# Performance work log

Hardware: AMD Instinct MI355X
Metric: run time of the kernel (lower is better)

## Reference

```python
import jax, jax.numpy as jnp
import numpy as np

E = 1024
BUCKET = 16
TAU = 0.75
ITERS = 8
SCALE = E ** -0.5
EPS = 1e-6


def _gumbel(rng, shape):
    u = jax.random.uniform(rng, shape, jnp.float32, 0.0, 1.0)
    return -jnp.log(-jnp.log(u + EPS) + EPS)


def _log_sinkhorn(log_alpha, n_iter):
    def body(i, la):
        la = la - jax.scipy.special.logsumexp(la, axis=-1, keepdims=True)
        la = la - jax.scipy.special.logsumexp(la, axis=-2, keepdims=True)
        return la
    return jnp.exp(jax.lax.fori_loop(0, n_iter, body, log_alpha))


def setup_inputs() -> dict:
    rng = jax.random.key(0)
    ks = jax.random.split(rng, 9)
    T, B, S = 4096, 8, 4096
    w = 0.02
    return {
        "query": jax.random.normal(ks[0], (T, B, E), jnp.float32),
        "key": jax.random.normal(ks[1], (S, B, E), jnp.float32),
        "value": jax.random.normal(ks[2], (S, B, E), jnp.float32),
        "wq": jax.random.normal(ks[3], (E, E), jnp.float32) * w,
        "bq": jnp.zeros((E,), jnp.float32),
        "wk": jax.random.normal(ks[4], (E, E), jnp.float32) * w,
        "bk": jnp.zeros((E,), jnp.float32),
        "wo": jax.random.normal(ks[5], (E, E), jnp.float32) * w,
        "bo": jnp.zeros((E,), jnp.float32),
    }


def reference(query, key, value, wq, bq, wk, bk, wo, bo):
    T, B, _ = query.shape
    S = key.shape[0]
    # projections (Linear: x @ W.T + b), move to (B, T, E)
    q = jnp.einsum('tbe,fe->btf', query, wq) + bq
    k = jnp.einsum('sbe,fe->bsf', key, wk) + bk
    v = jnp.transpose(value, (1, 0, 2))  # (B, S, E)
    nb, nkb = T // BUCKET, S // BUCKET
    # bucket aggregation: mean-pool q/k, flatten v buckets
    qb = q.reshape(B, nb, BUCKET, E).mean(axis=2)          # (B, nb, E)
    kb = k.reshape(B, nkb, BUCKET, E).mean(axis=2)         # (B, nkb, E)
    vb = v.reshape(B, nkb, BUCKET * E)                     # (B, nkb, BUCKET*E)
    # dot energy
    logits = jnp.einsum('bqe,bke->bqk', qb, kb) * SCALE    # (B, nb, nkb)
    log_alpha = logits
    # gumbel-sinkhorn (noise=True)
    g = _gumbel(jax.random.key(42), logits.shape)
    attn_weights = _log_sinkhorn((logits.astype(jnp.float32) + g) / TAU, ITERS)
    # attend on flattened buckets, then un-aggregate
    attn = jnp.einsum('bqk,bkd->bqd', attn_weights, vb)    # (B, nb, BUCKET*E)
    attn = attn.reshape(B, nb * BUCKET, E)
    attn = jnp.transpose(attn, (1, 0, 2))                  # (T, B, E)
    out = jnp.einsum('tbe,fe->tbf', attn, wo) + bo
    return out, attn_weights, log_alpha
```

## Files before the change

### kernel.cpp

```cpp
#include <hip/hip_runtime.h>


typedef float    f32x4 __attribute__((ext_vector_type(4)));
typedef _Float16 h4    __attribute__((ext_vector_type(4)));
typedef _Float16 h8    __attribute__((ext_vector_type(8)));

#define OUT_ELEMS 33554432
#define AW_ELEMS  524288

__device__ __forceinline__ void gload16(const void* g, void* l) {
  __builtin_amdgcn_global_load_lds((__attribute__((address_space(1))) void*)g,
                                   (__attribute__((address_space(3))) void*)l,
                                   16, 0, 0);
}

__global__ __launch_bounds__(256) void convw_k(const float* __restrict__ wq,
                                               const float* __restrict__ wk,
                                               const float* __restrict__ wo,
                                               _Float16* __restrict__ dst) {
  int which = blockIdx.y;
  const float* src = which == 0 ? wq : (which == 1 ? wk : wo);
  size_t idx = (size_t)blockIdx.x * 256 + threadIdx.x;
  f32x4 v = ((const f32x4*)src)[idx];
  ((h4*)(dst + (size_t)which * 1048576))[idx] = __builtin_convertvector(v, h4);
}

__global__ __launch_bounds__(256) void bucket_k(const float* __restrict__ q,
                                                const float* __restrict__ k,
                                                _Float16* __restrict__ qbar,
                                                _Float16* __restrict__ kbar) {
  const float* src = blockIdx.y ? k : q;
  _Float16* dst = blockIdx.y ? kbar : qbar;
  unsigned t = blockIdx.x * 256 + threadIdx.x;
  int e4 = t & 255, i = (t >> 8) & 255, b = t >> 16;
  const f32x4* p = (const f32x4*)(src + ((size_t)(i * 16) * 8 + b) * 1024) + e4;
  f32x4 acc = {0.f, 0.f, 0.f, 0.f};
  #pragma unroll
  for (int j = 0; j < 16; ++j) acc += p[j * 2048];
  acc *= 0.0625f;
  ((h4*)(dst + (size_t)(b * 256 + i) * 1024))[e4] = __builtin_convertvector(acc, h4);
}

__global__ __launch_bounds__(256) void vtrans_k(const float* __restrict__ v,
                                                _Float16* __restrict__ vt) {
  int bid = blockIdx.x;
  int kb = bid & 3, eb = (bid >> 2) & 15, j = (bid >> 6) & 15, b = bid >> 10;
  int k0 = kb * 64, e0 = eb * 64;
  __shared__ _Float16 tile[64][72];
  int t = threadIdx.x, r = t >> 2, qq = t & 3;
  const float* src = v + ((size_t)((k0 + r) * 16 + j) * 8 + b) * 1024 + e0;
  #pragma unroll
  for (int ii = 0; ii < 4; ++ii) {
    f32x4 x = ((const f32x4*)src)[qq + ii * 4];
    *(h4*)&tile[r][(qq + ii * 4) * 4] = __builtin_convertvector(x, h4);
  }
  __syncthreads();
  _Float16* dstp = vt + (((size_t)(b * 16 + j) * 1024 + e0 + r) * 256 + k0 + qq * 16);
  h8 o0, o1;
  #pragma unroll
  for (int kk = 0; kk < 8; ++kk) o0[kk] = tile[qq * 16 + kk][r];
  #pragma unroll
  for (int kk = 0; kk < 8; ++kk) o1[kk] = tile[qq * 16 + 8 + kk][r];
  *(h8*)dstp = o0;
  *(h8*)(dstp + 8) = o1;
}

__device__ __forceinline__ unsigned rotl32(unsigned x, int r) {
  return (x << r) | (x >> (32 - r));
}
__global__ __launch_bounds__(256) void gumbel_k(const float* __restrict__ logits,
                                                float* __restrict__ ebuf) {
  unsigned i = blockIdx.x * 256 + threadIdx.x;
  const unsigned k0 = 0u, k1 = 42u, k2 = 0u ^ 42u ^ 0x1BD11BDAu;
  unsigned x0 = 0u + k0, x1 = i + k1;
#define R4(a,b,c,d) \
  x0 += x1; x1 = rotl32(x1, a); x1 ^= x0; \
  x0 += x1; x1 = rotl32(x1, b); x1 ^= x0; \
  x0 += x1; x1 = rotl32(x1, c); x1 ^= x0; \
  x0 += x1; x1 = rotl32(x1, d); x1 ^= x0;
  R4(13,15,26,6)  x0 += k1; x1 += k2 + 1u;
  R4(17,29,16,24) x0 += k2; x1 += k0 + 2u;
  R4(13,15,26,6)  x0 += k0; x1 += k1 + 3u;
  R4(17,29,16,24) x0 += k1; x1 += k2 + 4u;
  R4(13,15,26,6)  x0 += k2; x1 += k0 + 5u;
#undef R4
  unsigned bits = x0 ^ x1;
  float u = __builtin_bit_cast(float, (bits >> 9) | 0x3f800000u) - 1.0f;
  float g = -logf(-logf(u + 1e-6f) + 1e-6f);
  ebuf[i] = __expf((logits[i] + g) / 0.75f);
}

__global__ __launch_bounds__(1024) void sink_rc_k(const float* __restrict__ ein,
                                                  float* __restrict__ attnw,
                                                  _Float16* __restrict__ wsh) {
  const int b = blockIdx.x;
  const int t = threadIdx.x;
  const int r = t >> 2, p = t & 3;
  const int k = t & 255, g = t >> 8;
  const float* Eb = ein + (size_t)b * 65536;
  const f32x4* Eb4 = (const f32x4*)Eb;

  __shared__ float ra[256];
  __shared__ float cb[256];
  __shared__ float part[4][256];
  if (t < 256) cb[t] = 1.0f;
  __syncthreads();

  const f32x4* cb4 = (const f32x4*)cb;

  for (int it = 0; it < 8; ++it) {
    float s = 0.f;
    #pragma unroll
    for (int i = 0; i < 16; ++i) {
      f32x4 e = Eb4[r * 64 + p * 16 + i];
      f32x4 c = cb4[p * 16 + i];
      f32x4 m = e * c;
      s += (m[0] + m[1]) + (m[2] + m[3]);
    }
    s += __shfl_xor(s, 1, 64);
    s += __shfl_xor(s, 2, 64);
    if (p == 0) ra[r] = 1.0f / s;
    __syncthreads();
    float s2 = 0.f;
    #pragma unroll 8
    for (int q2 = 0; q2 < 64; ++q2) {
      int row = g * 64 + q2;
      s2 += Eb[row * 256 + k] * ra[row];
    }
    part[g][k] = s2;
    __syncthreads();
    if (t < 256) {
      cb[t] = 1.0f / (part[0][t] + part[1][t] + part[2][t] + part[3][t]);
    }
    __syncthreads();
  }

  const float arow = ra[r];
  f32x4* aw = (f32x4*)(attnw + (size_t)b * 65536 + r * 256 + p * 64);
  h4* wh = (h4*)(wsh + (size_t)b * 65536 + r * 256 + p * 64);
  #pragma unroll
  for (int i = 0; i < 16; ++i) {
    f32x4 e = Eb4[r * 64 + p * 16 + i];
    f32x4 c = cb4[p * 16 + i];
    f32x4 w = e * c * arow;
    aw[i] = w;
    h4 hv;
    hv[0] = (_Float16)w[0]; hv[1] = (_Float16)w[1];
    hv[2] = (_Float16)w[2]; hv[3] = (_Float16)w[3];
    wh[i] = hv;
  }
}

template <int MODE>
__global__ __launch_bounds__(256) void gemm128(const _Float16* __restrict__ A,
                                               const _Float16* __restrict__ B,
                                               const float* __restrict__ bias,
                                               void* __restrict__ out0,
                                               int K, int lda, int ldb) {
  const int tid = threadIdx.x, lane = tid & 63, w = tid >> 6;
  int bx = blockIdx.x, by = blockIdx.y, bz = blockIdx.z;
  if constexpr (MODE == 0) {
    int wid = ((bx & 7) << 4) + (bx >> 3);
    by = wid & 7; bx = wid >> 3;
  }
  if constexpr (MODE == 2) {
    int wid = ((bx & 7) << 8) + (bx >> 3);
    bz = wid >> 4; by = (wid >> 1) & 7; bx = wid & 1;
  }
  if constexpr (MODE == 3) {
    int wid = ((bx & 7) << 8) + (bx >> 3);
    by = wid & 7; bx = wid >> 3;
  }
  const int m0 = bx * 128, n0 = by * 128;
  const _Float16* Ab = A;
  const _Float16* Bb = B;
  if constexpr (MODE == 1) { Ab += (size_t)bz * 262144; Bb += (size_t)bz * 262144; }
  if constexpr (MODE == 2) { Ab += (size_t)(bz >> 4) * 65536; Bb += (size_t)bz * 262144; }
  __shared__ _Float16 lA[128 * 32];
  __shared__ _Float16 lB[128 * 32];
  f32x4 acc[4][4] = {};
  const int wm = (w >> 1) * 64, wn = (w & 1) * 64;
  const int fr = lane & 15, fk = (lane >> 4) * 8;
  const int q0 = tid, q1 = tid + 256;

  for (int kt = 0; kt < K; kt += 32) {
    __syncthreads();
    gload16(Ab + (size_t)(m0 + (q0 >> 2)) * lda + kt + (q0 & 3) * 8, &lA[(w * 64) * 8]);
    gload16(Ab + (size_t)(m0 + (q1 >> 2)) * lda + kt + (q1 & 3) * 8, &lA[(256 + w * 64) * 8]);
    gload16(Bb + (size_t)(n0 + (q0 >> 2)) * ldb + kt + (q0 & 3) * 8, &lB[(w * 64) * 8]);
    gload16(Bb + (size_t)(n0 + (q1 >> 2)) * ldb + kt + (q1 & 3) * 8, &lB[(256 + w * 64) * 8]);
    __syncthreads();
    h8 af[4], bf[4];
    #pragma unroll
    for (int i = 0; i < 4; ++i) {
      af[i] = *(const h8*)&lA[(wm + i * 16 + fr) * 32 + fk];
      bf[i] = *(const h8*)&lB[(wn + i * 16 + fr) * 32 + fk];
    }
    #pragma unroll
    for (int mi = 0; mi < 4; ++mi)
      #pragma unroll
      for (int ni = 0; ni < 4; ++ni)
        acc[mi][ni] = __builtin_amdgcn_mfma_f32_16x16x32_f16(af[mi], bf[ni], acc[mi][ni], 0, 0, 0);
  }

  const int er = (lane >> 4) * 4;
  #pragma unroll
  for (int mi = 0; mi < 4; ++mi) {
    #pragma unroll
    for (int ni = 0; ni < 4; ++ni) {
      #pragma unroll
      for (int r = 0; r < 4; ++r) {
        int row = m0 + wm + mi * 16 + er + r;
        int col = n0 + wn + ni * 16 + fr;
        float val = acc[mi][ni][r];
        if constexpr (MODE == 0) {
          ((_Float16*)out0)[(size_t)row * 1024 + col] = (_Float16)(val + bias[col]);
        } else if constexpr (MODE == 1) {
          ((float*)out0)[(size_t)bz * 65536 + row * 256 + col] = val * 0.03125f;
        } else if constexpr (MODE == 2) {
          int b = bz >> 4, j = bz & 15;
          ((_Float16*)out0)[((size_t)(b * 4096 + row * 16 + j)) * 1024 + col] = (_Float16)val;
        } else {
          int bb = row >> 12, t = row & 4095;
          ((float*)out0)[((size_t)t * 8 + bb) * 1024 + col] = val + bias[col];
        }
      }
    }
  }
}

extern "C" void kernel_launch(void* const* d_in, const int* in_sizes, int n_in,
                              void* d_out, int out_size, void* d_ws, size_t ws_size,
                              hipStream_t stream) {
  const float* query = (const float*)d_in[0];
  const float* key   = (const float*)d_in[1];
  const float* value = (const float*)d_in[2];
  const float* wq    = (const float*)d_in[3];
  const float* bq    = (const float*)d_in[4];
  const float* wk    = (const float*)d_in[5];
  const float* bk    = (const float*)d_in[6];
  const float* wo    = (const float*)d_in[7];
  const float* bo    = (const float*)d_in[8];

  float* out      = (float*)d_out;
  float* attnw    = out + OUT_ELEMS;
  float* logalpha = out + OUT_ELEMS + AW_ELEMS;

  char* ws = (char*)d_ws;
  const size_t MB = 1024 * 1024;
  _Float16* wqh   = (_Float16*)(ws + 0 * MB);
  _Float16* wkh   = (_Float16*)(ws + 2 * MB);
  _Float16* woh   = (_Float16*)(ws + 4 * MB);
  _Float16* qbar  = (_Float16*)(ws + 6 * MB);
  _Float16* kbar  = (_Float16*)(ws + 10 * MB);
  _Float16* qbh   = (_Float16*)(ws + 14 * MB);
  _Float16* kbh   = (_Float16*)(ws + 18 * MB);
  float*    ebuf  = (float*)(ws + 22 * MB);
  _Float16* wsh   = (_Float16*)(ws + 25 * MB);
  _Float16* vt    = (_Float16*)(ws + 26 * MB);
  _Float16* attnh = (_Float16*)(ws + 90 * MB);
  (void)in_sizes; (void)n_in; (void)out_size; (void)ws_size;

  convw_k<<<dim3(1024, 3), 256, 0, stream>>>(wq, wk, wo, wqh);
  bucket_k<<<dim3(2048, 2), 256, 0, stream>>>(query, key, qbar, kbar);
  vtrans_k<<<dim3(8192), 256, 0, stream>>>(value, vt);

  gemm128<0><<<dim3(128), 256, 0, stream>>>(qbar, wqh, bq, qbh, 1024, 1024, 1024);
  gemm128<0><<<dim3(128), 256, 0, stream>>>(kbar, wkh, bk, kbh, 1024, 1024, 1024);
  gemm128<1><<<dim3(2, 2, 8), 256, 0, stream>>>(qbh, kbh, nullptr, logalpha, 1024, 1024, 1024);

  gumbel_k<<<dim3(2048), 256, 0, stream>>>(logalpha, ebuf);
  sink_rc_k<<<dim3(8), 1024, 0, stream>>>(ebuf, attnw, wsh);

  gemm128<2><<<dim3(2048), 256, 0, stream>>>(wsh, vt, nullptr, attnh, 256, 256, 256);
  gemm128<3><<<dim3(2048), 256, 0, stream>>>(attnh, woh, bo, out, 1024, 1024, 1024);
}
```

Before: 400.1 us.

## Reassociate output projection: project value by Wo first, then apply attention weights

Uses associativity to compute V·Wo^T directly from fp32 value (converting to fp16 on the fly in the loader), then multiplies the Sinkhorn weights by the projected values and adds bias in the final kernel. This removes the separate value-transpose kernel and the large intermediate attention buffer, replacing two GEMMs with two of the same size. The final kernel transposes VW tiles into LDS with scalar stores, which may cause bank conflicts, and the precision path changes because VW is rounded to fp16 before the attention multiply.

```diff
diff --git a/kernel.cpp b/kernel.cpp
--- a/kernel.cpp
+++ b/kernel.cpp
@@ -39,30 +39,6 @@
   for (int j = 0; j < 16; ++j) acc += p[j * 2048];
   acc *= 0.0625f;
   ((h4*)(dst + (size_t)(b * 256 + i) * 1024))[e4] = __builtin_convertvector(acc, h4);
-}
-
-__global__ __launch_bounds__(256) void vtrans_k(const float* __restrict__ v,
-                                                _Float16* __restrict__ vt) {
-  int bid = blockIdx.x;
-  int kb = bid & 3, eb = (bid >> 2) & 15, j = (bid >> 6) & 15, b = bid >> 10;
-  int k0 = kb * 64, e0 = eb * 64;
-  __shared__ _Float16 tile[64][72];
-  int t = threadIdx.x, r = t >> 2, qq = t & 3;
-  const float* src = v + ((size_t)((k0 + r) * 16 + j) * 8 + b) * 1024 + e0;
-  #pragma unroll
-  for (int ii = 0; ii < 4; ++ii) {
-    f32x4 x = ((const f32x4*)src)[qq + ii * 4];
-    *(h4*)&tile[r][(qq + ii * 4) * 4] = __builtin_convertvector(x, h4);
-  }
-  __syncthreads();
-  _Float16* dstp = vt + (((size_t)(b * 16 + j) * 1024 + e0 + r) * 256 + k0 + qq * 16);
-  h8 o0, o1;
-  #pragma unroll
-  for (int kk = 0; kk < 8; ++kk) o0[kk] = tile[qq * 16 + kk][r];
-  #pragma unroll
-  for (int kk = 0; kk < 8; ++kk) o1[kk] = tile[qq * 16 + 8 + kk][r];
-  *(h8*)dstp = o0;
-  *(h8*)(dstp + 8) = o1;
 }
 
 __device__ __forceinline__ unsigned rotl32(unsigned x, int r) {
@@ -163,19 +139,10 @@
     int wid = ((bx & 7) << 4) + (bx >> 3);
     by = wid & 7; bx = wid >> 3;
   }
-  if constexpr (MODE == 2) {
-    int wid = ((bx & 7) << 8) + (bx >> 3);
-    bz = wid >> 4; by = (wid >> 1) & 7; bx = wid & 1;
-  }
-  if constexpr (MODE == 3) {
-    int wid = ((bx & 7) << 8) + (bx >> 3);
-    by = wid & 7; bx = wid >> 3;
-  }
   const int m0 = bx * 128, n0 = by * 128;
   const _Float16* Ab = A;
   const _Float16* Bb = B;
   if constexpr (MODE == 1) { Ab += (size_t)bz * 262144; Bb += (size_t)bz * 262144; }
-  if constexpr (MODE == 2) { Ab += (size_t)(bz >> 4) * 65536; Bb += (size_t)bz * 262144; }
   __shared__ _Float16 lA[128 * 32];
   __shared__ _Float16 lB[128 * 32];
   f32x4 acc[4][4] = {};
@@ -215,18 +182,122 @@
         float val = acc[mi][ni][r];
         if constexpr (MODE == 0) {
           ((_Float16*)out0)[(size_t)row * 1024 + col] = (_Float16)(val + bias[col]);
-        } else if constexpr (MODE == 1) {
+        } else {
           ((float*)out0)[(size_t)bz * 65536 + row * 256 + col] = val * 0.03125f;
-        } else if constexpr (MODE == 2) {
-          int b = bz >> 4, j = bz & 15;
-          ((_Float16*)out0)[((size_t)(b * 4096 + row * 16 + j)) * 1024 + col] = (_Float16)val;
-        } else {
-          int bb = row >> 12, t = row & 4095;
-          ((float*)out0)[((size_t)t * 8 + bb) * 1024 + col] = val + bias[col];
         }
       }
     }
   }
+}
+
+__global__ __launch_bounds__(256) void vproj_k(const float* __restrict__ V,
+                                               const _Float16* __restrict__ woh,
+                                               _Float16* __restrict__ VW) {
+  const int tid = threadIdx.x, lane = tid & 63, w = tid >> 6;
+  int bx = blockIdx.x;
+  int wid = ((bx & 7) << 8) + (bx >> 3);
+  const int m0 = (wid >> 3) * 128, n0 = (wid & 7) * 128;
+  __shared__ _Float16 lA[128 * 32];
+  __shared__ _Float16 lB[128 * 32];
+  f32x4 acc[4][4] = {};
+  const int wm = (w >> 1) * 64, wn = (w & 1) * 64;
+  const int fr = lane & 15, fk = (lane >> 4) * 8;
+  const int q0 = tid, q1 = tid + 256;
+  const int ar = tid >> 3, ae = (tid & 7) * 4;
+
+  for (int kt = 0; kt < 1024; kt += 32) {
+    __syncthreads();
+    #pragma unroll
+    for (int p = 0; p < 4; ++p) {
+      int row = p * 32 + ar;
+      f32x4 x = *(const f32x4*)(V + (size_t)(m0 + row) * 1024 + kt + ae);
+      *(h4*)&lA[row * 32 + ae] = __builtin_convertvector(x, h4);
+    }
+    gload16(woh + (size_t)(n0 + (q0 >> 2)) * 1024 + kt + (q0 & 3) * 8, &lB[(w * 64) * 8]);
+    gload16(woh + (size_t)(n0 + (q1 >> 2)) * 1024 + kt + (q1 & 3) * 8, &lB[(256 + w * 64) * 8]);
+    __syncthreads();
+    h8 af[4], bf[4];
+    #pragma unroll
+    for (int i = 0; i < 4; ++i) {
+      af[i] = *(const h8*)&lA[(wm + i * 16 + fr) * 32 + fk];
+      bf[i] = *(const h8*)&lB[(wn + i * 16 + fr) * 32 + fk];
+    }
+    #pragma unroll
+    for (int mi = 0; mi < 4; ++mi)
+      #pragma unroll
+      for (int ni = 0; ni < 4; ++ni)
+        acc[mi][ni] = __builtin_amdgcn_mfma_f32_16x16x32_f16(af[mi], bf[ni], acc[mi][ni], 0, 0, 0);
+  }
+
+  const int er = (lane >> 4) * 4;
+  #pragma unroll
+  for (int mi = 0; mi < 4; ++mi)
+    #pragma unroll
+    for (int ni = 0; ni < 4; ++ni)
+      #pragma unroll
+      for (int r = 0; r < 4; ++r) {
+        int row = m0 + wm + mi * 16 + er + r;
+        int col = n0 + wn + ni * 16 + fr;
+        VW[(size_t)row * 1024 + col] = (_Float16)acc[mi][ni][r];
+      }
+}
+
+__global__ __launch_bounds__(256) void fin_k(const _Float16* __restrict__ wsh,
+                                             const _Float16* __restrict__ VW,
+                                             const float* __restrict__ bo,
+                                             float* __restrict__ out) {
+  const int tid = threadIdx.x, lane = tid & 63, w = tid >> 6;
+  int bx = blockIdx.x;
+  int wid = ((bx & 7) << 8) + (bx >> 3);
+  const int bj = wid >> 4, mt = (wid >> 3) & 1, nt = wid & 7;
+  const int b = bj & 7, j = bj >> 3;
+  const int m0 = mt * 128, n0 = nt * 128;
+  const _Float16* Ab = wsh + (size_t)b * 65536;
+  __shared__ _Float16 lA[128 * 32];
+  __shared__ _Float16 lB[128 * 40];
+  f32x4 acc[4][4] = {};
+  const int wm = (w >> 1) * 64, wn = (w & 1) * 64;
+  const int fr = lane & 15, fk = (lane >> 4) * 8;
+  const int q0 = tid, q1 = tid + 256;
+  const int bk = tid >> 3, bf0 = (tid & 7) * 8;
+
+  for (int kt = 0; kt < 256; kt += 32) {
+    __syncthreads();
+    gload16(Ab + (size_t)(m0 + (q0 >> 2)) * 256 + kt + (q0 & 3) * 8, &lA[(w * 64) * 8]);
+    gload16(Ab + (size_t)(m0 + (q1 >> 2)) * 256 + kt + (q1 & 3) * 8, &lA[(256 + w * 64) * 8]);
+    #pragma unroll
+    for (int half = 0; half < 2; ++half) {
+      int f0 = bf0 + half * 64;
+      int vrow = (kt + bk) * 128 + j * 8 + b;
+      h8 v = *(const h8*)(VW + (size_t)vrow * 1024 + n0 + f0);
+      #pragma unroll
+      for (int u = 0; u < 8; ++u) lB[(f0 + u) * 40 + bk] = v[u];
+    }
+    __syncthreads();
+    h8 af[4], bfv[4];
+    #pragma unroll
+    for (int i = 0; i < 4; ++i) {
+      af[i] = *(const h8*)&lA[(wm + i * 16 + fr) * 32 + fk];
+      bfv[i] = *(const h8*)&lB[(wn + i * 16 + fr) * 40 + fk];
+    }
+    #pragma unroll
+    for (int mi = 0; mi < 4; ++mi)
+      #pragma unroll
+      for (int ni = 0; ni < 4; ++ni)
+        acc[mi][ni] = __builtin_amdgcn_mfma_f32_16x16x32_f16(af[mi], bfv[ni], acc[mi][ni], 0, 0, 0);
+  }
+
+  const int er = (lane >> 4) * 4;
+  #pragma unroll
+  for (int mi = 0; mi < 4; ++mi)
+    #pragma unroll
+    for (int ni = 0; ni < 4; ++ni)
+      #pragma unroll
+      for (int r = 0; r < 4; ++r) {
+        int row = m0 + wm + mi * 16 + er + r;
+        int col = n0 + wn + ni * 16 + fr;
+        out[((size_t)(row * 16 + j) * 8 + b) * 1024 + col] = acc[mi][ni][r] + bo[col];
+      }
 }
 
 extern "C" void kernel_launch(void* const* d_in, const int* in_sizes, int n_in,
@@ -257,13 +328,13 @@
   _Float16* kbh   = (_Float16*)(ws + 18 * MB);
   float*    ebuf  = (float*)(ws + 22 * MB);
   _Float16* wsh   = (_Float16*)(ws + 25 * MB);
-  _Float16* vt    = (_Float16*)(ws + 26 * MB);
-  _Float16* attnh = (_Float16*)(ws + 90 * MB);
+  _Float16* VW    = (_Float16*)(ws + 26 * MB);
   (void)in_sizes; (void)n_in; (void)out_size; (void)ws_size;
 
   convw_k<<<dim3(1024, 3), 256, 0, stream>>>(wq, wk, wo, wqh);
   bucket_k<<<dim3(2048, 2), 256, 0, stream>>>(query, key, qbar, kbar);
-  vtrans_k<<<dim3(8192), 256, 0, stream>>>(value, vt);
+
+  vproj_k<<<dim3(2048), 256, 0, stream>>>(value, woh, VW);
 
   gemm128<0><<<dim3(128), 256, 0, stream>>>(qbar, wqh, bq, qbh, 1024, 1024, 1024);
   gemm128<0><<<dim3(128), 256, 0, stream>>>(kbar, wkh, bk, kbh, 1024, 1024, 1024);
@@ -272,6 +343,5 @@
   gumbel_k<<<dim3(2048), 256, 0, stream>>>(logalpha, ebuf);
   sink_rc_k<<<dim3(8), 1024, 0, stream>>>(ebuf, attnw, wsh);
 
-  gemm128<2><<<dim3(2048), 256, 0, stream>>>(wsh, vt, nullptr, attnh, 256, 256, 256);
-  gemm128<3><<<dim3(2048), 256, 0, stream>>>(attnh, woh, bo, out, 1024, 1024, 1024);
-}
+  fin_k<<<dim3(2048), 256, 0, stream>>>(wsh, VW, bo, out);
+}
```

Result: slower. 415.3 us (+3.8%).
